# Performance work log

Measured on AMD Instinct MI355X. Metric: run time of the kernel, lower is better.

The kernel has to match this reference:

```python
import jax, jax.numpy as jnp
import numpy as np

B, P, NB, WN, CI, CO = 4, 20000, 9, 17, 64, 128

def setup_inputs() -> dict:
    key = jax.random.key(0)
    k0, k1, k2, k3 = jax.random.split(key, 4)
    in_pc = jax.random.normal(k0, (B, P, CI), dtype=jnp.float32)
    raw_w_weights = jax.random.normal(k1, (P, NB, WN), dtype=jnp.float32) * 0.1
    # padded/missing neighbors use id == P, which indexes the zero-pad row and is masked
    neighbor_ids = jax.random.randint(k2, (P, NB), 0, P + 1)
    weights = jax.random.normal(k3, (WN, CO * CI), dtype=jnp.float32)
    bias = jnp.zeros((P, CO), dtype=jnp.float32)
    return {"in_pc": in_pc, "raw_w_weights": raw_w_weights, "weights": weights,
            "bias": bias, "neighbor_ids": neighbor_ids}

def reference(in_pc, raw_w_weights, weights, bias, neighbor_ids):
    b, p, ci = in_pc.shape
    wn = weights.shape[0]
    co = bias.shape[-1]
    # pc_mask: 1 for real points, 0 for the pad row (id == in_pn)
    nb_mask = (neighbor_ids < p).astype(in_pc.dtype)          # [p, nb]
    w_weights = raw_w_weights * nb_mask[:, :, None]           # [p, nb, wn]
    in_pc_pad = jnp.concatenate(
        [in_pc, jnp.zeros((b, 1, ci), dtype=in_pc.dtype)], axis=1)  # [b, p+1, ci]
    in_neighbors = in_pc_pad[:, neighbor_ids]                 # [b, p, nb, ci] gather
    # weighted fuse over neighbors into wn basis slots
    fuse = jnp.einsum('pnm,bpni->bpmi', w_weights, in_neighbors)   # [b, p, wn, ci]
    Wm = weights.reshape(wn, co, ci)
    # per-basis conv then sum-reduce over wn (b_max_pool=False), fused into one einsum
    out_pc = jnp.einsum('moi,bpmi->bpo', Wm, fuse) + bias      # [b, p, co]
    # is_final_layer=False -> ELU; residual_rate=0 -> no residual branch
    return jax.nn.elu(out_pc)
```

## Files before the change

### kernel.cpp

```cpp
#include <hip/hip_runtime.h>
#include <stdint.h>

#define B_   4
#define P_   20000
#define NB_  9
#define WN_  17
#define CI_  64
#define CO_  128
#define PTS  16
#define NBLK (P_ / PTS)

typedef __fp16 f16x8 __attribute__((ext_vector_type(8)));
typedef __fp16 h2    __attribute__((ext_vector_type(2)));
typedef float  f32x16 __attribute__((ext_vector_type(16)));

union H2U { h2 h; uint32_t u; };
union F8U { f16x8 v; h2 h[4]; uint4 u; };

__global__ void prep_wm(const float* __restrict__ w, ushort* __restrict__ wsb) {
    int i = blockIdx.x * 256 + threadIdx.x;
    int m2p  = i >> 9;
    int r    = i & 511;
    int oloc = r >> 7, co = r & 127;
    int m = m2p >> 1, p = m2p & 1;
    const float* src = w + (size_t)m * (CO_ * CI_) + co * CI_ + (p * 4 + oloc) * 8;
    float4 v0 = *(const float4*)(src);
    float4 v1 = *(const float4*)(src + 4);
    F8U h;
    h.h[0] = __builtin_amdgcn_cvt_pkrtz(v0.x, v0.y);
    h.h[1] = __builtin_amdgcn_cvt_pkrtz(v0.z, v0.w);
    h.h[2] = __builtin_amdgcn_cvt_pkrtz(v1.x, v1.y);
    h.h[3] = __builtin_amdgcn_cvt_pkrtz(v1.z, v1.w);
    *(uint4*)&wsb[(size_t)((m2p * 4 + oloc) * 128 + co) * 8] = h.u;
}

template <bool PRE>
__global__ __launch_bounds__(256, 3)
void lasm_fused(const float* __restrict__ in_pc,
                const float* __restrict__ raw_w,
                const float* __restrict__ weights,
                const float* __restrict__ bias,
                const int*   __restrict__ nbr,
                const ushort* __restrict__ wsb,
                float*       __restrict__ out)
{
    __shared__ __align__(16) int      s_nid[PTS * NB_];
    __shared__ __align__(16) uint32_t s_w2[WN_ * NB_ * 17];

    const int tid  = threadIdx.x;
    const int lane = tid & 63;
    const int wv   = tid >> 6;
    const int arow = lane & 31;
    const int q    = lane >> 5;
    const int mt   = wv >> 1;
    const int ch   = wv & 1;
    const int p0   = blockIdx.x * PTS;

    if (tid < PTS * NB_) s_nid[tid] = nbr[p0 * NB_ + tid];
    for (int idx = tid; idx < PTS * NB_ * WN_; idx += 256) {
        int pl2 = idx / (NB_ * WN_);
        int rem = idx % (NB_ * WN_);
        int n   = rem / WN_;
        int m   = rem % WN_;
        float wf = raw_w[(size_t)p0 * NB_ * WN_ + idx];
        H2U c; c.h = __builtin_amdgcn_cvt_pkrtz(wf, wf);
        s_w2[(m * NB_ + n) * 17 + pl2] = c.u;
    }
    __syncthreads();

    f32x16 acc[2];
    #pragma unroll
    for (int c = 0; c < 2; ++c)
        #pragma unroll
        for (int j = 0; j < 16; ++j) acc[c][j] = 0.f;

    const int brow = mt * 2 + (arow >> 4);
    const int pl   = arow & 15;
    const size_t binpc = (size_t)brow * P_ * CI_;

    auto load_b = [&](int m, int pass, int kk, int c) -> f16x8 {
        int oloc = kk * 2 + q;
        if (PRE) {
            F8U r;
            r.u = *(const uint4*)&wsb[(size_t)(((m * 2 + pass) * 4 + oloc) * 128
                                               + ch * 64 + c * 32 + arow) * 8];
            return r.v;
        } else {
            const float* s = weights + (size_t)m * (CO_ * CI_)
                           + (ch * 64 + c * 32 + arow) * CI_ + (pass * 4 + oloc) * 8;
            float4 v0 = *(const float4*)(s);
            float4 v1 = *(const float4*)(s + 4);
            F8U r;
            r.h[0] = __builtin_amdgcn_cvt_pkrtz(v0.x, v0.y);
            r.h[1] = __builtin_amdgcn_cvt_pkrtz(v0.z, v0.w);
            r.h[2] = __builtin_amdgcn_cvt_pkrtz(v1.x, v1.y);
            r.h[3] = __builtin_amdgcn_cvt_pkrtz(v1.z, v1.w);
            return r.v;
        }
    };

    for (int pass = 0; pass < 2; ++pass) {
        h2 x[NB_][8];
        const int ch0 = pass * 32 + q * 8;
        #pragma unroll
        for (int n = 0; n < NB_; ++n) {
            uint32_t nid = (uint32_t)s_nid[pl * NB_ + n];
            if (nid < (uint32_t)P_) {
                const float* src = in_pc + binpc + (size_t)nid * CI_ + ch0;
                float4 a0 = *(const float4*)(src);
                float4 a1 = *(const float4*)(src + 4);
                float4 b0 = *(const float4*)(src + 16);
                float4 b1 = *(const float4*)(src + 20);
                x[n][0] = __builtin_amdgcn_cvt_pkrtz(a0.x, a0.y);
                x[n][1] = __builtin_amdgcn_cvt_pkrtz(a0.z, a0.w);
                x[n][2] = __builtin_amdgcn_cvt_pkrtz(a1.x, a1.y);
                x[n][3] = __builtin_amdgcn_cvt_pkrtz(a1.z, a1.w);
                x[n][4] = __builtin_amdgcn_cvt_pkrtz(b0.x, b0.y);
                x[n][5] = __builtin_amdgcn_cvt_pkrtz(b0.z, b0.w);
                x[n][6] = __builtin_amdgcn_cvt_pkrtz(b1.x, b1.y);
                x[n][7] = __builtin_amdgcn_cvt_pkrtz(b1.z, b1.w);
            } else {
                h2 z = {(__fp16)0.f, (__fp16)0.f};
                #pragma unroll
                for (int j = 0; j < 8; ++j) x[n][j] = z;
            }
        }

        f16x8 bA0 = load_b(0, pass, 0, 0);
        f16x8 bA1 = load_b(0, pass, 0, 1);

        for (int m = 0; m < WN_; ++m) {
            H2U wc[9];
            #pragma unroll
            for (int n = 0; n < NB_; ++n) wc[n].u = s_w2[(m * NB_ + n) * 17 + pl];

            F8U f[2];
            #pragma unroll
            for (int kk = 0; kk < 2; ++kk) {
                #pragma unroll
                for (int r4 = 0; r4 < 4; ++r4) {
                    h2 c = {(__fp16)0.f, (__fp16)0.f};
                    #pragma unroll
                    for (int n = 0; n < NB_; ++n) c += wc[n].h * x[n][kk * 4 + r4];
                    f[kk].h[r4] = c;
                }
            }

            f16x8 bB0 = load_b(m, pass, 1, 0);
            f16x8 bB1 = load_b(m, pass, 1, 1);
            acc[0] = __builtin_amdgcn_mfma_f32_32x32x16_f16(f[0].v, bA0, acc[0], 0, 0, 0);
            acc[1] = __builtin_amdgcn_mfma_f32_32x32x16_f16(f[0].v, bA1, acc[1], 0, 0, 0);

            int mn = (m + 1 < WN_) ? m + 1 : m;
            f16x8 nA0 = load_b(mn, pass, 0, 0);
            f16x8 nA1 = load_b(mn, pass, 0, 1);
            acc[0] = __builtin_amdgcn_mfma_f32_32x32x16_f16(f[1].v, bB0, acc[0], 0, 0, 0);
            acc[1] = __builtin_amdgcn_mfma_f32_32x32x16_f16(f[1].v, bB1, acc[1], 0, 0, 0);
            bA0 = nA0; bA1 = nA1;
        }
    }

    #pragma unroll
    for (int c = 0; c < 2; ++c) {
        int col = ch * 64 + c * 32 + arow;
        #pragma unroll
        for (int v = 0; v < 16; ++v) {
            int lr = (v & 3) + 8 * (v >> 2) + 4 * q;
            int b  = mt * 2 + (lr >> 4);
            int p  = p0 + (lr & 15);
            float val = acc[c][v] + bias[(size_t)p * CO_ + col];
            val = (val > 0.f) ? val : (__expf(val) - 1.f);
            __builtin_nontemporal_store(val, &out[((size_t)b * P_ + p) * CO_ + col]);
        }
    }
}

extern "C" void kernel_launch(void* const* d_in, const int* in_sizes, int n_in,
                              void* d_out, int out_size, void* d_ws, size_t ws_size,
                              hipStream_t stream) {
    const float* in_pc   = (const float*)d_in[0];
    const float* raw_w   = (const float*)d_in[1];
    const float* weights = (const float*)d_in[2];
    const float* bias    = (const float*)d_in[3];
    const int*   nbr     = (const int*)  d_in[4];
    float* out = (float*)d_out;

    const size_t need = (size_t)WN_ * 2 * 4096 * sizeof(ushort);
    if (d_ws != nullptr && ws_size >= need) {
        ushort* wsb = (ushort*)d_ws;
        prep_wm<<<dim3(WN_ * 2 * 512 / 256), dim3(256), 0, stream>>>(weights, wsb);
        lasm_fused<true><<<dim3(NBLK), dim3(256), 0, stream>>>(
            in_pc, raw_w, weights, bias, nbr, wsb, out);
    } else {
        lasm_fused<false><<<dim3(NBLK), dim3(256), 0, stream>>>(
            in_pc, raw_w, weights, bias, nbr, nullptr, out);
    }
}
```

Measured before the change: 168.8 us.

## Remap waves to one batch each with 32 points and all output channels

Each block now handles 32 points instead of 16, and each wave owns one batch and all 128 output channels. Before, each wave handled two batches for half the channels, so the neighbor fuse was computed twice per point. Now the fuse is computed once and used by four MFMAs, and neighbor ids are loaded straight into registers instead of staged through LDS. The first gather is issued before the raw-weight LDS fill so the two overlap. In exchange register pressure rises (four accumulators), occupancy drops to 2 blocks per SM, and the block count halves, which leaves fewer blocks to spread across the GPU.

```diff
diff --git a/kernel.cpp b/kernel.cpp
--- a/kernel.cpp
+++ b/kernel.cpp
@@ -7,7 +7,7 @@
 #define WN_  17
 #define CI_  64
 #define CO_  128
-#define PTS  16
+#define PTS  32
 #define NBLK (P_ / PTS)
 
 typedef __fp16 f16x8 __attribute__((ext_vector_type(8)));
@@ -35,7 +35,7 @@
 }
 
 template <bool PRE>
-__global__ __launch_bounds__(256, 3)
+__global__ __launch_bounds__(256, 2)
 void lasm_fused(const float* __restrict__ in_pc,
                 const float* __restrict__ raw_w,
                 const float* __restrict__ weights,
@@ -44,69 +44,29 @@
                 const ushort* __restrict__ wsb,
                 float*       __restrict__ out)
 {
-    __shared__ __align__(16) int      s_nid[PTS * NB_];
-    __shared__ __align__(16) uint32_t s_w2[WN_ * NB_ * 17];
+    __shared__ __align__(16) uint32_t s_w2[WN_ * NB_ * 33];
 
     const int tid  = threadIdx.x;
     const int lane = tid & 63;
     const int wv   = tid >> 6;
     const int arow = lane & 31;
     const int q    = lane >> 5;
-    const int mt   = wv >> 1;
-    const int ch   = wv & 1;
     const int p0   = blockIdx.x * PTS;
 
-    if (tid < PTS * NB_) s_nid[tid] = nbr[p0 * NB_ + tid];
-    for (int idx = tid; idx < PTS * NB_ * WN_; idx += 256) {
-        int pl2 = idx / (NB_ * WN_);
-        int rem = idx % (NB_ * WN_);
-        int n   = rem / WN_;
-        int m   = rem % WN_;
-        float wf = raw_w[(size_t)p0 * NB_ * WN_ + idx];
-        H2U c; c.h = __builtin_amdgcn_cvt_pkrtz(wf, wf);
-        s_w2[(m * NB_ + n) * 17 + pl2] = c.u;
-    }
-    __syncthreads();
-
-    f32x16 acc[2];
+    int nid[NB_];
     #pragma unroll
-    for (int c = 0; c < 2; ++c)
-        #pragma unroll
-        for (int j = 0; j < 16; ++j) acc[c][j] = 0.f;
-
-    const int brow = mt * 2 + (arow >> 4);
-    const int pl   = arow & 15;
-    const size_t binpc = (size_t)brow * P_ * CI_;
-
-    auto load_b = [&](int m, int pass, int kk, int c) -> f16x8 {
-        int oloc = kk * 2 + q;
-        if (PRE) {
-            F8U r;
-            r.u = *(const uint4*)&wsb[(size_t)(((m * 2 + pass) * 4 + oloc) * 128
-                                               + ch * 64 + c * 32 + arow) * 8];
-            return r.v;
-        } else {
-            const float* s = weights + (size_t)m * (CO_ * CI_)
-                           + (ch * 64 + c * 32 + arow) * CI_ + (pass * 4 + oloc) * 8;
-            float4 v0 = *(const float4*)(s);
-            float4 v1 = *(const float4*)(s + 4);
-            F8U r;
-            r.h[0] = __builtin_amdgcn_cvt_pkrtz(v0.x, v0.y);
-            r.h[1] = __builtin_amdgcn_cvt_pkrtz(v0.z, v0.w);
-            r.h[2] = __builtin_amdgcn_cvt_pkrtz(v1.x, v1.y);
-            r.h[3] = __builtin_amdgcn_cvt_pkrtz(v1.z, v1.w);
-            return r.v;
-        }
-    };
-
-    for (int pass = 0; pass < 2; ++pass) {
-        h2 x[NB_][8];
+    for (int n = 0; n < NB_; ++n)
+        nid[n] = nbr[(size_t)(p0 + arow) * NB_ + n];
+
+    const size_t binpc = (size_t)wv * P_ * CI_;
+
+    h2 x[NB_][8];
+    auto gather = [&](int pass) {
         const int ch0 = pass * 32 + q * 8;
         #pragma unroll
         for (int n = 0; n < NB_; ++n) {
-            uint32_t nid = (uint32_t)s_nid[pl * NB_ + n];
-            if (nid < (uint32_t)P_) {
-                const float* src = in_pc + binpc + (size_t)nid * CI_ + ch0;
+            if ((uint32_t)nid[n] < (uint32_t)P_) {
+                const float* src = in_pc + binpc + (size_t)nid[n] * CI_ + ch0;
                 float4 a0 = *(const float4*)(src);
                 float4 a1 = *(const float4*)(src + 4);
                 float4 b0 = *(const float4*)(src + 16);
@@ -125,52 +85,106 @@
                 for (int j = 0; j < 8; ++j) x[n][j] = z;
             }
         }
-
-        f16x8 bA0 = load_b(0, pass, 0, 0);
-        f16x8 bA1 = load_b(0, pass, 0, 1);
+    };
+
+    gather(0);
+
+    for (int idx = tid; idx < PTS * NB_ * WN_; idx += 256) {
+        int pl2 = idx / (NB_ * WN_);
+        int rem = idx % (NB_ * WN_);
+        int n   = rem / WN_;
+        int m   = rem % WN_;
+        float wf = raw_w[(size_t)p0 * NB_ * WN_ + idx];
+        H2U c; c.h = __builtin_amdgcn_cvt_pkrtz(wf, wf);
+        s_w2[(m * NB_ + n) * 33 + pl2] = c.u;
+    }
+    __syncthreads();
+
+    f32x16 acc[4];
+    #pragma unroll
+    for (int c = 0; c < 4; ++c)
+        #pragma unroll
+        for (int j = 0; j < 16; ++j) acc[c][j] = 0.f;
+
+    auto load_b = [&](int m, int pass, int kk, int c) -> f16x8 {
+        int oloc = kk * 2 + q;
+        if (PRE) {
+            F8U r;
+            r.u = *(const uint4*)&wsb[(size_t)(((m * 2 + pass) * 4 + oloc) * 128
+                                               + c * 32 + arow) * 8];
+            return r.v;
+        } else {
+            const float* s = weights + (size_t)m * (CO_ * CI_)
+                           + (c * 32 + arow) * CI_ + (pass * 4 + oloc) * 8;
+            float4 v0 = *(const float4*)(s);
+            float4 v1 = *(const float4*)(s + 4);
+            F8U r;
+            r.h[0] = __builtin_amdgcn_cvt_pkrtz(v0.x, v0.y);
+            r.h[1] = __builtin_amdgcn_cvt_pkrtz(v0.z, v0.w);
+            r.h[2] = __builtin_amdgcn_cvt_pkrtz(v1.x, v1.y);
+            r.h[3] = __builtin_amdgcn_cvt_pkrtz(v1.z, v1.w);
+            return r.v;
+        }
+    };
+
+    auto mloop = [&](int pass) {
+        f16x8 bA[4];
+        #pragma unroll
+        for (int c = 0; c < 4; ++c) bA[c] = load_b(0, pass, 0, c);
 
         for (int m = 0; m < WN_; ++m) {
-            H2U wc[9];
-            #pragma unroll
-            for (int n = 0; n < NB_; ++n) wc[n].u = s_w2[(m * NB_ + n) * 17 + pl];
+            H2U wc[NB_];
+            #pragma unroll
+            for (int n = 0; n < NB_; ++n) wc[n].u = s_w2[(m * NB_ + n) * 33 + arow];
 
             F8U f[2];
             #pragma unroll
             for (int kk = 0; kk < 2; ++kk) {
                 #pragma unroll
                 for (int r4 = 0; r4 < 4; ++r4) {
-                    h2 c = {(__fp16)0.f, (__fp16)0.f};
+                    h2 c2 = {(__fp16)0.f, (__fp16)0.f};
                     #pragma unroll
-                    for (int n = 0; n < NB_; ++n) c += wc[n].h * x[n][kk * 4 + r4];
-                    f[kk].h[r4] = c;
+                    for (int n = 0; n < NB_; ++n) c2 += wc[n].h * x[n][kk * 4 + r4];
+                    f[kk].h[r4] = c2;
                 }
             }
 
-            f16x8 bB0 = load_b(m, pass, 1, 0);
-            f16x8 bB1 = load_b(m, pass, 1, 1);
-            acc[0] = __builtin_amdgcn_mfma_f32_32x32x16_f16(f[0].v, bA0, acc[0], 0, 0, 0);
-            acc[1] = __builtin_amdgcn_mfma_f32_32x32x16_f16(f[0].v, bA1, acc[1], 0, 0, 0);
+            f16x8 bB[4];
+            #pragma unroll
+            for (int c = 0; c < 4; ++c) bB[c] = load_b(m, pass, 1, c);
+
+            #pragma unroll
+            for (int c = 0; c < 4; ++c)
+                acc[c] = __builtin_amdgcn_mfma_f32_32x32x16_f16(f[0].v, bA[c], acc[c], 0, 0, 0);
 
             int mn = (m + 1 < WN_) ? m + 1 : m;
-            f16x8 nA0 = load_b(mn, pass, 0, 0);
-            f16x8 nA1 = load_b(mn, pass, 0, 1);
-            acc[0] = __builtin_amdgcn_mfma_f32_32x32x16_f16(f[1].v, bB0, acc[0], 0, 0, 0);
-            acc[1] = __builtin_amdgcn_mfma_f32_32x32x16_f16(f[1].v, bB1, acc[1], 0, 0, 0);
-            bA0 = nA0; bA1 = nA1;
-        }
-    }
+            f16x8 nA[4];
+            #pragma unroll
+            for (int c = 0; c < 4; ++c) nA[c] = load_b(mn, pass, 0, c);
+
+            #pragma unroll
+            for (int c = 0; c < 4; ++c)
+                acc[c] = __builtin_amdgcn_mfma_f32_32x32x16_f16(f[1].v, bB[c], acc[c], 0, 0, 0);
+
+            #pragma unroll
+            for (int c = 0; c < 4; ++c) bA[c] = nA[c];
+        }
+    };
+
+    mloop(0);
+    gather(1);
+    mloop(1);
 
     #pragma unroll
-    for (int c = 0; c < 2; ++c) {
-        int col = ch * 64 + c * 32 + arow;
+    for (int c = 0; c < 4; ++c) {
+        int col = c * 32 + arow;
         #pragma unroll
         for (int v = 0; v < 16; ++v) {
             int lr = (v & 3) + 8 * (v >> 2) + 4 * q;
-            int b  = mt * 2 + (lr >> 4);
-            int p  = p0 + (lr & 15);
+            int p  = p0 + lr;
             float val = acc[c][v] + bias[(size_t)p * CO_ + col];
             val = (val > 0.f) ? val : (__expf(val) - 1.f);
-            __builtin_nontemporal_store(val, &out[((size_t)b * P_ + p) * CO_ + col]);
+            __builtin_nontemporal_store(val, &out[((size_t)wv * P_ + p) * CO_ + col]);
         }
     }
 }
```

New measurement: 167.1 us. About the same (-1.0%).

## Split CI into four 16-wide slices to shrink gather registers and reorder weights

Applied to the files above, without the earlier changes.

The channel loop now runs in four 16-channel slices instead of two 32-channel passes. Each slice gathers only 8 channels per neighbor, which halves the x register array, and issues one MFMA pair per basis slot. Neighbor ids now live in registers instead of shared memory, the first gather is issued before the raw-weight staging to overlap its latency, and the prepped fp16 weights are laid out slice-major to match. The change trades lower register pressure, and possibly higher occupancy, for twice as many outer iterations and the loss of the previous B-operand prefetch.

```diff
diff --git a/kernel.cpp b/kernel.cpp
--- a/kernel.cpp
+++ b/kernel.cpp
@@ -19,11 +19,12 @@
 
 __global__ void prep_wm(const float* __restrict__ w, ushort* __restrict__ wsb) {
     int i = blockIdx.x * 256 + threadIdx.x;
-    int m2p  = i >> 9;
-    int r    = i & 511;
-    int oloc = r >> 7, co = r & 127;
-    int m = m2p >> 1, p = m2p & 1;
-    const float* src = w + (size_t)m * (CO_ * CI_) + co * CI_ + (p * 4 + oloc) * 8;
+    int co = i & 127;
+    int t  = i >> 7;
+    int q  = t & 1;  t >>= 1;
+    int m  = t % WN_;
+    int s  = t / WN_;
+    const float* src = w + (size_t)m * (CO_ * CI_) + co * CI_ + s * 16 + q * 8;
     float4 v0 = *(const float4*)(src);
     float4 v1 = *(const float4*)(src + 4);
     F8U h;
@@ -31,7 +32,7 @@
     h.h[1] = __builtin_amdgcn_cvt_pkrtz(v0.z, v0.w);
     h.h[2] = __builtin_amdgcn_cvt_pkrtz(v1.x, v1.y);
     h.h[3] = __builtin_amdgcn_cvt_pkrtz(v1.z, v1.w);
-    *(uint4*)&wsb[(size_t)((m2p * 4 + oloc) * 128 + co) * 8] = h.u;
+    *(uint4*)&wsb[(size_t)i * 8] = h.u;
 }
 
 template <bool PRE>
@@ -44,7 +45,6 @@
                 const ushort* __restrict__ wsb,
                 float*       __restrict__ out)
 {
-    __shared__ __align__(16) int      s_nid[PTS * NB_];
     __shared__ __align__(16) uint32_t s_w2[WN_ * NB_ * 17];
 
     const int tid  = threadIdx.x;
@@ -55,8 +55,37 @@
     const int mt   = wv >> 1;
     const int ch   = wv & 1;
     const int p0   = blockIdx.x * PTS;
+    const int pl   = arow & 15;
+    const int brow = mt * 2 + (arow >> 4);
+    const size_t binpc = (size_t)brow * P_ * CI_;
 
-    if (tid < PTS * NB_) s_nid[tid] = nbr[p0 * NB_ + tid];
+    uint32_t nid[NB_];
+    #pragma unroll
+    for (int n = 0; n < NB_; ++n)
+        nid[n] = (uint32_t)nbr[(size_t)(p0 + pl) * NB_ + n];
+
+    h2 x[NB_][4];
+    auto gather = [&](int s) {
+        const int ch0 = s * 16 + q * 8;
+        #pragma unroll
+        for (int n = 0; n < NB_; ++n) {
+            if (nid[n] < (uint32_t)P_) {
+                const float* src = in_pc + binpc + (size_t)nid[n] * CI_ + ch0;
+                float4 a0 = *(const float4*)(src);
+                float4 a1 = *(const float4*)(src + 4);
+                x[n][0] = __builtin_amdgcn_cvt_pkrtz(a0.x, a0.y);
+                x[n][1] = __builtin_amdgcn_cvt_pkrtz(a0.z, a0.w);
+                x[n][2] = __builtin_amdgcn_cvt_pkrtz(a1.x, a1.y);
+                x[n][3] = __builtin_amdgcn_cvt_pkrtz(a1.z, a1.w);
+            } else {
+                h2 z = {(__fp16)0.f, (__fp16)0.f};
+                #pragma unroll
+                for (int j = 0; j < 4; ++j) x[n][j] = z;
+            }
+        }
+    };
+
+    gather(0);
     for (int idx = tid; idx < PTS * NB_ * WN_; idx += 256) {
         int pl2 = idx / (NB_ * WN_);
         int rem = idx % (NB_ * WN_);
@@ -68,107 +97,65 @@
     }
     __syncthreads();
 
-    f32x16 acc[2];
+    f32x16 acc0, acc1;
     #pragma unroll
-    for (int c = 0; c < 2; ++c)
+    for (int j = 0; j < 16; ++j) { acc0[j] = 0.f; acc1[j] = 0.f; }
+
+    for (int s = 0; s < 4; ++s) {
+        if (s) gather(s);
         #pragma unroll
-        for (int j = 0; j < 16; ++j) acc[c][j] = 0.f;
-
-    const int brow = mt * 2 + (arow >> 4);
-    const int pl   = arow & 15;
-    const size_t binpc = (size_t)brow * P_ * CI_;
-
-    auto load_b = [&](int m, int pass, int kk, int c) -> f16x8 {
-        int oloc = kk * 2 + q;
-        if (PRE) {
-            F8U r;
-            r.u = *(const uint4*)&wsb[(size_t)(((m * 2 + pass) * 4 + oloc) * 128
-                                               + ch * 64 + c * 32 + arow) * 8];
-            return r.v;
-        } else {
-            const float* s = weights + (size_t)m * (CO_ * CI_)
-                           + (ch * 64 + c * 32 + arow) * CI_ + (pass * 4 + oloc) * 8;
-            float4 v0 = *(const float4*)(s);
-            float4 v1 = *(const float4*)(s + 4);
-            F8U r;
-            r.h[0] = __builtin_amdgcn_cvt_pkrtz(v0.x, v0.y);
-            r.h[1] = __builtin_amdgcn_cvt_pkrtz(v0.z, v0.w);
-            r.h[2] = __builtin_amdgcn_cvt_pkrtz(v1.x, v1.y);
-            r.h[3] = __builtin_amdgcn_cvt_pkrtz(v1.z, v1.w);
-            return r.v;
-        }
-    };
-
-    for (int pass = 0; pass < 2; ++pass) {
-        h2 x[NB_][8];
-        const int ch0 = pass * 32 + q * 8;
-        #pragma unroll
-        for (int n = 0; n < NB_; ++n) {
-            uint32_t nid = (uint32_t)s_nid[pl * NB_ + n];
-            if (nid < (uint32_t)P_) {
-                const float* src = in_pc + binpc + (size_t)nid * CI_ + ch0;
-                float4 a0 = *(const float4*)(src);
-                float4 a1 = *(const float4*)(src + 4);
-                float4 b0 = *(const float4*)(src + 16);
-                float4 b1 = *(const float4*)(src + 20);
-                x[n][0] = __builtin_amdgcn_cvt_pkrtz(a0.x, a0.y);
-                x[n][1] = __builtin_amdgcn_cvt_pkrtz(a0.z, a0.w);
-                x[n][2] = __builtin_amdgcn_cvt_pkrtz(a1.x, a1.y);
-                x[n][3] = __builtin_amdgcn_cvt_pkrtz(a1.z, a1.w);
-                x[n][4] = __builtin_amdgcn_cvt_pkrtz(b0.x, b0.y);
-                x[n][5] = __builtin_amdgcn_cvt_pkrtz(b0.z, b0.w);
-                x[n][6] = __builtin_amdgcn_cvt_pkrtz(b1.x, b1.y);
-                x[n][7] = __builtin_amdgcn_cvt_pkrtz(b1.z, b1.w);
-            } else {
-                h2 z = {(__fp16)0.f, (__fp16)0.f};
-                #pragma unroll
-                for (int j = 0; j < 8; ++j) x[n][j] = z;
-            }
-        }
-
-        f16x8 bA0 = load_b(0, pass, 0, 0);
-        f16x8 bA1 = load_b(0, pass, 0, 1);
-
         for (int m = 0; m < WN_; ++m) {
-            H2U wc[9];
+            H2U wc[NB_];
             #pragma unroll
             for (int n = 0; n < NB_; ++n) wc[n].u = s_w2[(m * NB_ + n) * 17 + pl];
 
-            F8U f[2];
+            F8U fa;
             #pragma unroll
-            for (int kk = 0; kk < 2; ++kk) {
+            for (int r4 = 0; r4 < 4; ++r4) {
+                h2 c2 = {(__fp16)0.f, (__fp16)0.f};
                 #pragma unroll
-                for (int r4 = 0; r4 < 4; ++r4) {
-                    h2 c = {(__fp16)0.f, (__fp16)0.f};
-                    #pragma unroll
-                    for (int n = 0; n < NB_; ++n) c += wc[n].h * x[n][kk * 4 + r4];
-                    f[kk].h[r4] = c;
-                }
+                for (int n = 0; n < NB_; ++n) c2 += wc[n].h * x[n][r4];
+                fa.h[r4] = c2;
             }
 
-            f16x8 bB0 = load_b(m, pass, 1, 0);
-            f16x8 bB1 = load_b(m, pass, 1, 1);
-            acc[0] = __builtin_amdgcn_mfma_f32_32x32x16_f16(f[0].v, bA0, acc[0], 0, 0, 0);
-            acc[1] = __builtin_amdgcn_mfma_f32_32x32x16_f16(f[0].v, bA1, acc[1], 0, 0, 0);
+            F8U b0, b1;
+            if (PRE) {
+                const size_t gb = ((size_t)((s * WN_ + m) * 2 + q) * 128
+                                   + ch * 64 + arow) * 8;
+                b0.u = *(const uint4*)&wsb[gb];
+                b1.u = *(const uint4*)&wsb[gb + 32 * 8];
+            } else {
+                const float* sp = weights + (size_t)m * (CO_ * CI_)
+                                + (ch * 64 + arow) * CI_ + s * 16 + q * 8;
+                float4 v0 = *(const float4*)(sp);
+                float4 v1 = *(const float4*)(sp + 4);
+                b0.h[0] = __builtin_amdgcn_cvt_pkrtz(v0.x, v0.y);
+                b0.h[1] = __builtin_amdgcn_cvt_pkrtz(v0.z, v0.w);
+                b0.h[2] = __builtin_amdgcn_cvt_pkrtz(v1.x, v1.y);
+                b0.h[3] = __builtin_amdgcn_cvt_pkrtz(v1.z, v1.w);
+                const float* sp1 = sp + 32 * CI_;
+                float4 w0 = *(const float4*)(sp1);
+                float4 w1 = *(const float4*)(sp1 + 4);
+                b1.h[0] = __builtin_amdgcn_cvt_pkrtz(w0.x, w0.y);
+                b1.h[1] = __builtin_amdgcn_cvt_pkrtz(w0.z, w0.w);
+                b1.h[2] = __builtin_amdgcn_cvt_pkrtz(w1.x, w1.y);
+                b1.h[3] = __builtin_amdgcn_cvt_pkrtz(w1.z, w1.w);
+            }
 
-            int mn = (m + 1 < WN_) ? m + 1 : m;
-            f16x8 nA0 = load_b(mn, pass, 0, 0);
-            f16x8 nA1 = load_b(mn, pass, 0, 1);
-            acc[0] = __builtin_amdgcn_mfma_f32_32x32x16_f16(f[1].v, bB0, acc[0], 0, 0, 0);
-            acc[1] = __builtin_amdgcn_mfma_f32_32x32x16_f16(f[1].v, bB1, acc[1], 0, 0, 0);
-            bA0 = nA0; bA1 = nA1;
+            acc0 = __builtin_amdgcn_mfma_f32_32x32x16_f16(fa.v, b0.v, acc0, 0, 0, 0);
+            acc1 = __builtin_amdgcn_mfma_f32_32x32x16_f16(fa.v, b1.v, acc1, 0, 0, 0);
         }
     }
 
     #pragma unroll
     for (int c = 0; c < 2; ++c) {
-        int col = ch * 64 + c * 32 + arow;
+        const int col = ch * 64 + c * 32 + arow;
         #pragma unroll
         for (int v = 0; v < 16; ++v) {
             int lr = (v & 3) + 8 * (v >> 2) + 4 * q;
             int b  = mt * 2 + (lr >> 4);
             int p  = p0 + (lr & 15);
-            float val = acc[c][v] + bias[(size_t)p * CO_ + col];
+            float val = (c == 0 ? acc0[v] : acc1[v]) + bias[(size_t)p * CO_ + col];
             val = (val > 0.f) ? val : (__expf(val) - 1.f);
             __builtin_nontemporal_store(val, &out[((size_t)b * P_ + p) * CO_ + col]);
         }
@@ -185,10 +172,10 @@
     const int*   nbr     = (const int*)  d_in[4];
     float* out = (float*)d_out;
 
-    const size_t need = (size_t)WN_ * 2 * 4096 * sizeof(ushort);
+    const size_t need = (size_t)4 * WN_ * 2 * 128 * 8 * sizeof(ushort);
     if (d_ws != nullptr && ws_size >= need) {
         ushort* wsb = (ushort*)d_ws;
-        prep_wm<<<dim3(WN_ * 2 * 512 / 256), dim3(256), 0, stream>>>(weights, wsb);
+        prep_wm<<<dim3(68), dim3(256), 0, stream>>>(weights, wsb);
         lasm_fused<true><<<dim3(NBLK), dim3(256), 0, stream>>>(
             in_pc, raw_w, weights, bias, nbr, wsb, out);
     } else {
```

Result: slower. 359.0 us (+112.7%).
